# Performance work log

Hardware: AMD Instinct MI355X
Metric: run time of the kernel (lower is better)

The kernel has to match this reference:

```python
import jax, jax.numpy as jnp
import numpy as np

B, L, D = 2, 2048, 2048
H, KVH, Dh = 16, 8, 128
S_ROPE = 1024
EPS = 1e-5


def rms_norm(x, w):
    xf = x.astype(jnp.float32)
    xf = xf * jax.lax.rsqrt(jnp.mean(xf * xf, axis=-1, keepdims=True) + EPS)
    return (xf * w).astype(x.dtype)


def rotate_half(x):
    x1, x2 = jnp.split(x, 2, axis=-1)
    return jnp.concatenate((-x2, x1), axis=-1)


def setup_inputs() -> dict:
    key = jax.random.key(0)
    ks = jax.random.split(key, 12)
    sc = 0.02
    # 1D rope tables at every absolute position (theta = 500000 as in config)
    inv_freq = 1.0 / (500000.0 ** (np.arange(0, Dh, 2, dtype=np.float32) / Dh))
    ang = np.arange(L, dtype=np.float32)[:, None] * inv_freq[None, :]  # [L, Dh/2]
    emb = np.concatenate([ang, ang], axis=-1)  # [L, Dh]
    # 3D rope as per-pair 2x2 rotation matrices
    ang3 = np.random.RandomState(0).uniform(-np.pi, np.pi, size=(S_ROPE, Dh // 2)).astype(np.float32)
    R = np.stack([np.stack([np.cos(ang3), -np.sin(ang3)], -1),
                  np.stack([np.sin(ang3), np.cos(ang3)], -1)], -2)  # [S,Dh/2,2,2]
    mpos = jnp.array([[[128, 1025], [1160, 513]],
                      [[128, 1025], [1160, 513]]], dtype=jnp.int64)
    return {
        "hidden_states": jax.random.normal(ks[0], (B, L, D), jnp.float32),
        "temb": jax.random.normal(ks[1], (B, D), jnp.float32),
        "w_ln": jnp.ones((D,), jnp.float32),
        "w_mod": jax.random.normal(ks[2], (D, 3 * D), jnp.float32) * sc,
        "b_mod": jnp.zeros((3 * D,), jnp.float32),
        "wq": jax.random.normal(ks[3], (D, H * Dh), jnp.float32) * sc,
        "wk": jax.random.normal(ks[4], (D, KVH * Dh), jnp.float32) * sc,
        "wv": jax.random.normal(ks[5], (D, KVH * Dh), jnp.float32) * sc,
        "wo": jax.random.normal(ks[6], (H * Dh, D), jnp.float32) * sc,
        "qn_w": jnp.ones((Dh,), jnp.float32),
        "kn_w": jnp.ones((Dh,), jnp.float32),
        "cos_1d": jnp.asarray(np.cos(emb)),
        "sin_1d": jnp.asarray(np.sin(emb)),
        "rope_3d": jnp.asarray(R),
        "modality_positions": mpos,
    }


def _masks(modality_positions):
    pos = jnp.arange(L)  # [L]
    off = modality_positions[..., 0]   # [B, S]
    ln = modality_positions[..., 1]    # [B, S]
    meta = 1  # add_time_embeds=True, add_ar_embeds=False
    seg_end = off + jnp.maximum(ln, meta)
    in_full = (pos[None, None, :] >= off[..., None]) & (pos[None, None, :] < seg_end[..., None])
    text_mask = ~jnp.any(in_full, axis=1)  # [B, L]
    img_start = off + meta
    in_img = (pos[None, None, :] >= img_start[..., None]) & (pos[None, None, :] < (off + ln)[..., None])
    rel = jnp.sum(jnp.where(in_img, pos[None, None, :] - img_start[..., None], 0), axis=1)  # [B, L]
    img_mask = jnp.any(in_img, axis=1) & (rel < S_ROPE) & (rel >= 0)
    rel = jnp.clip(rel, 0, S_ROPE - 1)
    return text_mask, img_mask, rel


def _apply_mixed_rope(q, k, cos_1d, sin_1d, rope_3d, text_mask, img_mask, rel):
    # text 1D rope (rotate_half style), applied at absolute position
    c = cos_1d[None, None]  # [1,1,L,Dh]
    s = sin_1d[None, None]
    q_txt = q * c + rotate_half(q) * s
    k_txt = k * c + rotate_half(k) * s
    # image 3D rope: per-pair 2x2 rotation gathered at within-image index
    R = rope_3d[rel]  # [B, L, Dh/2, 2, 2]
    q2 = q.reshape(*q.shape[:-1], Dh // 2, 2)
    k2 = k.reshape(*k.shape[:-1], Dh // 2, 2)
    q_img = jnp.einsum('bhlpi,blpij->bhlpj', q2, R).reshape(q.shape)
    k_img = jnp.einsum('bhlpi,blpij->bhlpj', k2, R).reshape(k.shape)
    mt = text_mask[:, None, :, None]
    mi = img_mask[:, None, :, None]
    q_out = jnp.where(mt, q_txt, jnp.where(mi, q_img, q))
    k_out = jnp.where(mt, k_txt, jnp.where(mi, k_img, k))
    return q_out, k_out


def reference(hidden_states, temb, w_ln, w_mod, b_mod, wq, wk, wv, wo,
              qn_w, kn_w, cos_1d, sin_1d, rope_3d, modality_positions):
    dtype = hidden_states.dtype
    # adaLN modulation
    mod = jax.nn.silu(temb) @ w_mod + b_mod  # [B, 3D]
    shift, scale, gate = jnp.split(mod, 3, axis=-1)
    xn = rms_norm(hidden_states, w_ln)
    xm = (xn.astype(jnp.float32) * (1.0 + scale[:, None, :].astype(jnp.float32))
          + shift[:, None, :].astype(jnp.float32)).astype(dtype)
    # qkv projections (GQA)
    q = (xm @ wq).reshape(B, L, H, Dh).transpose(0, 2, 1, 3)
    k = (xm @ wk).reshape(B, L, KVH, Dh).transpose(0, 2, 1, 3)
    v = (xm @ wv).reshape(B, L, KVH, Dh).transpose(0, 2, 1, 3)
    # qk-norm over head_dim
    q = rms_norm(q, qn_w)
    k = rms_norm(k, kn_w)
    # mixed 3D-image / 1D-text RoPE
    text_mask, img_mask, rel = _masks(modality_positions)
    q, k = _apply_mixed_rope(q, k, cos_1d, sin_1d, rope_3d, text_mask, img_mask, rel)
    # GQA: repeat kv heads (repeat_interleave along head dim)
    n_rep = H // KVH
    k = jnp.repeat(k, n_rep, axis=1)
    v = jnp.repeat(v, n_rep, axis=1)
    # full attention (no causal mask for diffusion block)
    scores = jnp.einsum('bhqd,bhkd->bhqk', q, k) / jnp.sqrt(jnp.asarray(Dh, q.dtype))
    attn = jax.nn.softmax(scores, axis=-1)
    o = jnp.einsum('bhqk,bhkd->bhqd', attn, v)
    o = o.transpose(0, 2, 1, 3).reshape(B, L, H * Dh) @ wo
    return hidden_states + gate[:, None, :].astype(dtype) * o


if __name__ == '__main__':
    out = reference(**setup_inputs())
    print(out.shape, out.dtype)
```

## Files before the change

### kernel.cpp

```cpp
#include <hip/hip_runtime.h>
#include <stdint.h>
#include <math.h>

typedef unsigned short u16;
typedef __attribute__((ext_vector_type(8))) short short8;
typedef __attribute__((ext_vector_type(4))) float fx4;
typedef __attribute__((ext_vector_type(4))) unsigned short u16x4;

#define DEV __device__ __forceinline__

DEV u16 f2bf(float f) {
  unsigned u = __builtin_bit_cast(unsigned, f);
  return (u16)((u + 0x7FFFu + ((u >> 16) & 1u)) >> 16);
}
DEV float bf2f(u16 h) { return __builtin_bit_cast(float, ((unsigned)h) << 16); }

DEV fx4 mfma16(short8 a, short8 b, fx4 c) {
  return __builtin_amdgcn_mfma_f32_16x16x32_bf16(a, b, c, 0, 0, 0);
}

#define GLD16(g, l)                                                            \
  __builtin_amdgcn_global_load_lds(                                            \
      (const __attribute__((address_space(1))) void*)(g),                      \
      (__attribute__((address_space(3))) void*)(l), 16, 0, 0)

__global__ __launch_bounds__(512) void k_silu_mod(
    const float* __restrict__ temb, const float* __restrict__ wmod,
    const float* __restrict__ bmod, float* __restrict__ mod) {
  __shared__ float st[4096];
  __shared__ float red[8][2][64];
  int tid = threadIdx.x;
  for (int i = tid; i < 4096; i += 512) {
    float t = temb[i];
    st[i] = t / (1.0f + __expf(-t));
  }
  __syncthreads();
  int j = blockIdx.x * 64 + (tid & 63);
  int ks = tid >> 6;
  float a0 = 0.f, a1 = 0.f;
  for (int d = ks * 256; d < ks * 256 + 256; ++d) {
    float w = wmod[(size_t)d * 6144 + j];
    a0 += st[d] * w;
    a1 += st[2048 + d] * w;
  }
  red[ks][0][tid & 63] = a0;
  red[ks][1][tid & 63] = a1;
  __syncthreads();
  if (tid < 64) {
    float s0 = 0.f, s1 = 0.f;
#pragma unroll
    for (int i = 0; i < 8; ++i) {
      s0 += red[i][0][tid];
      s1 += red[i][1][tid];
    }
    mod[j] = s0 + bmod[j];
    mod[6144 + j] = s1 + bmod[j];
  }
}

__global__ __launch_bounds__(256) void k_xm(
    const float* __restrict__ x, const float* __restrict__ wln,
    const float* __restrict__ mod, u16* __restrict__ xm) {
  int row = blockIdx.x;
  int b = row >> 11;
  const float* xr = x + (size_t)row * 2048;
  int tid = threadIdx.x;
  float4 v0 = ((const float4*)xr)[tid];
  float4 v1 = ((const float4*)xr)[tid + 256];
  float ss = v0.x * v0.x + v0.y * v0.y + v0.z * v0.z + v0.w * v0.w +
             v1.x * v1.x + v1.y * v1.y + v1.z * v1.z + v1.w * v1.w;
  for (int m = 1; m < 64; m <<= 1) ss += __shfl_xor(ss, m);
  __shared__ float red[4];
  if ((tid & 63) == 0) red[tid >> 6] = ss;
  __syncthreads();
  ss = red[0] + red[1] + red[2] + red[3];
  float r = rsqrtf(ss * (1.0f / 2048.0f) + 1e-5f);
  const float* mb = mod + (size_t)b * 6144;
#pragma unroll
  for (int c = 0; c < 2; ++c) {
    int j0 = (tid + c * 256) * 4;
    float4 xv = c ? v1 : v0;
    float4 sh = *(const float4*)(mb + j0);
    float4 sc = *(const float4*)(mb + 2048 + j0);
    float4 wl = *(const float4*)(wln + j0);
    u16x4 o;
    o.x = f2bf(xv.x * r * wl.x * (1.f + sc.x) + sh.x);
    o.y = f2bf(xv.y * r * wl.y * (1.f + sc.y) + sh.y);
    o.z = f2bf(xv.z * r * wl.z * (1.f + sc.z) + sh.z);
    o.w = f2bf(xv.w * r * wl.w * (1.f + sc.w) + sh.w);
    *(u16x4*)(xm + (size_t)row * 2048 + j0) = o;
  }
}

__global__ __launch_bounds__(256) void k_tconv(
    const float* __restrict__ src, u16* __restrict__ dst, int cols, int rows) {
  __shared__ float t[32][33];
  int kb = blockIdx.x * 32, nb = blockIdx.y * 32;
  int tx = threadIdx.x, ty = threadIdx.y;
#pragma unroll
  for (int i = 0; i < 4; ++i)
    t[ty + i * 8][tx] = src[(size_t)(kb + ty + i * 8) * cols + nb + tx];
  __syncthreads();
#pragma unroll
  for (int i = 0; i < 4; ++i)
    dst[(size_t)(nb + ty + i * 8) * rows + kb + tx] = f2bf(t[tx][ty + i * 8]);
}

template <int EPI>
__global__ __launch_bounds__(256) void k_gemm(
    const u16* __restrict__ A, const u16* __restrict__ Bt, void* __restrict__ Cp,
    const float* __restrict__ hid, const float* __restrict__ mod, int N, int K) {
  __shared__ u16 As[128 * 32];
  __shared__ u16 Bs[128 * 32];
  int tid = threadIdx.x;
  int wave = tid >> 6, lane = tid & 63, quad = lane >> 4, l16 = lane & 15;
  int m0 = blockIdx.y * 128, n0 = blockIdx.x * 128;
  int wm = (wave >> 1) * 64, wn = (wave & 1) * 64;
  fx4 acc[4][4] = {};
  int rowa = tid >> 2;
  int chunk = (tid & 3) ^ ((rowa >> 1) & 3);
  int cola = chunk * 8;
  const u16* Ag = A + (size_t)(m0 + rowa) * K + cola;
  const u16* Bg = Bt + (size_t)(n0 + rowa) * K + cola;
  u16* AsW = &As[wave * 512];
  u16* BsW = &Bs[wave * 512];
  int sl = (quad ^ ((l16 >> 1) & 3)) * 8;
  for (int k0 = 0; k0 < K; k0 += 32) {
    GLD16(Ag + k0, AsW);
    GLD16(Ag + k0 + (size_t)64 * K, AsW + 2048);
    GLD16(Bg + k0, BsW);
    GLD16(Bg + k0 + (size_t)64 * K, BsW + 2048);
    __syncthreads();
    short8 af[4], bfr[4];
#pragma unroll
    for (int i = 0; i < 4; ++i) {
      af[i] = *(const short8*)&As[(wm + i * 16 + l16) * 32 + sl];
      bfr[i] = *(const short8*)&Bs[(wn + i * 16 + l16) * 32 + sl];
    }
#pragma unroll
    for (int i = 0; i < 4; ++i)
#pragma unroll
      for (int j = 0; j < 4; ++j) acc[i][j] = mfma16(af[i], bfr[j], acc[i][j]);
    __syncthreads();
  }
#pragma unroll
  for (int i = 0; i < 4; ++i) {
    int row = m0 + wm + i * 16 + quad * 4;
#pragma unroll
    for (int j = 0; j < 4; ++j) {
      int col = n0 + wn + j * 16 + l16;
      if (EPI == 0) {
        u16* C = (u16*)Cp;
#pragma unroll
        for (int r = 0; r < 4; ++r)
          C[(size_t)(row + r) * N + col] = f2bf(acc[i][j][r]);
      } else {
        float* C = (float*)Cp;
        int b = row >> 11;
        float g = mod[(size_t)b * 6144 + 4096 + col];
#pragma unroll
        for (int r = 0; r < 4; ++r)
          C[(size_t)(row + r) * N + col] =
              hid[(size_t)(row + r) * N + col] + g * acc[i][j][r];
      }
    }
  }
}

__global__ __launch_bounds__(192) void k_qknorm(
    const u16* __restrict__ qkv, const float* __restrict__ qn,
    const float* __restrict__ kn, const float* __restrict__ cos1,
    const float* __restrict__ sin1, const float* __restrict__ r3,
    const int* __restrict__ mpos, u16* __restrict__ Q, u16* __restrict__ Kb) {
  int bx = blockIdx.x;
  int b = bx >> 11, l = bx & 2047;
  int tid = threadIdx.x;
  int slot = tid >> 3, sub = tid & 7;
  bool isq = slot < 16;
  int head = isq ? slot : slot - 16;
  const u16* base = qkv + (size_t)bx * 4096 + (isq ? slot * 128 : 2048 + head * 128);
  int d0 = sub * 16;
  float xv[16];
#pragma unroll
  for (int i = 0; i < 16; ++i) xv[i] = bf2f(base[d0 + i]);
  float ss = 0.f;
#pragma unroll
  for (int i = 0; i < 16; ++i) ss += xv[i] * xv[i];
  ss += __shfl_xor(ss, 1);
  ss += __shfl_xor(ss, 2);
  ss += __shfl_xor(ss, 4);
  float r = rsqrtf(ss * (1.0f / 128.0f) + 1e-5f);
  int mp[8];
  {
    bool is64 = (mpos[1] == 0) & (mpos[3] == 0) & (mpos[5] == 0) & (mpos[7] == 0);
#pragma unroll
    for (int i = 0; i < 8; ++i) mp[i] = is64 ? mpos[2 * i] : mpos[i];
  }
  bool infull = false, inimg = false;
  int rel = 0;
#pragma unroll
  for (int s = 0; s < 2; ++s) {
    int off = mp[b * 4 + s * 2], ln = mp[b * 4 + s * 2 + 1];
    int mx = ln > 1 ? ln : 1;
    infull |= (l >= off) && (l < off + mx);
    bool ii = (l >= off + 1) && (l < off + ln);
    inimg |= ii;
    rel += ii ? (l - (off + 1)) : 0;
  }
  bool text = !infull;
  bool img = inimg && (rel < 1024);
  const float* w = isq ? qn : kn;
  float out[16];
  if (text) {
    int dp0 = d0 ^ 64;
    float sgn = (d0 < 64) ? -1.f : 1.f;
#pragma unroll
    for (int i = 0; i < 16; ++i) {
      int d = d0 + i, dp = dp0 + i;
      float c = cos1[(size_t)l * 128 + d];
      float s = sin1[(size_t)l * 128 + d];
      float xp = bf2f(base[dp]);
      out[i] = r * (xv[i] * w[d] * c + sgn * xp * w[dp] * s);
    }
  } else if (img) {
    const float* R = r3 + ((size_t)rel * 64 + (d0 >> 1)) * 4;
#pragma unroll
    for (int p = 0; p < 8; ++p) {
      float a = xv[2 * p] * w[d0 + 2 * p] * r;
      float c2 = xv[2 * p + 1] * w[d0 + 2 * p + 1] * r;
      out[2 * p] = a * R[4 * p + 0] + c2 * R[4 * p + 2];
      out[2 * p + 1] = a * R[4 * p + 1] + c2 * R[4 * p + 3];
    }
  } else {
#pragma unroll
    for (int i = 0; i < 16; ++i) out[i] = xv[i] * w[d0 + i] * r;
  }
  if (isq) {
    u16* dst = Q + ((size_t)(b * 16 + head) * 2048 + l) * 128 + d0;
#pragma unroll
    for (int i = 0; i < 16; ++i) dst[i] = f2bf(out[i] * 0.08838834764831845f);
  } else {
    u16* dst = Kb + ((size_t)(b * 8 + head) * 2048 + l) * 128 + d0;
#pragma unroll
    for (int i = 0; i < 16; ++i) dst[i] = f2bf(out[i]);
  }
}

__global__ __launch_bounds__(256) void k_vtrans(const u16* __restrict__ qkv,
                                                u16* __restrict__ VT) {
  __shared__ u16 t[64][65];
  int bh = blockIdx.x;
  int l0 = blockIdx.y * 64, d0 = blockIdx.z * 64;
  int b = bh >> 3, kvh = bh & 7;
  int tx = threadIdx.x & 63, tg = threadIdx.x >> 6;
#pragma unroll
  for (int i = 0; i < 16; ++i) {
    int li = tg + i * 4;
    t[li][tx] = qkv[(size_t)(b * 2048 + l0 + li) * 4096 + 3072 + kvh * 128 + d0 + tx];
  }
  __syncthreads();
#pragma unroll
  for (int i = 0; i < 16; ++i) {
    int di = tg + i * 4;
    VT[((size_t)bh * 128 + d0 + di) * 2048 + l0 + tx] = t[tx][di];
  }
}

__global__ __launch_bounds__(256, 4) void k_attn(
    const u16* __restrict__ Q, const u16* __restrict__ Kb,
    const u16* __restrict__ VT, u16* __restrict__ O) {
  __shared__ u16 Ks[64 * 128];
  __shared__ u16 Vs[128 * 64];
  __shared__ u16 Ps[64 * 64];
  int tid = threadIdx.x;
  int wave = tid >> 6, lane = tid & 63, quad = lane >> 4, l16 = lane & 15;
  int bh = blockIdx.y;
  int b = bh >> 4, h = bh & 15, kvh = h >> 1;
  int q0 = blockIdx.x * 64;
  const u16* Qb = Q + ((size_t)bh * 2048 + q0 + wave * 16) * 128;
  short8 qf[4];
#pragma unroll
  for (int ks = 0; ks < 4; ++ks)
    qf[ks] = *(const short8*)(Qb + l16 * 128 + ks * 32 + quad * 8);
  const u16* Kg = Kb + (size_t)(b * 8 + kvh) * 2048 * 128;
  const u16* Vg = VT + (size_t)(b * 8 + kvh) * 128 * 2048;
  float mrow[4], lrow[4];
  fx4 of[8] = {};
#pragma unroll
  for (int r = 0; r < 4; ++r) {
    mrow[r] = -INFINITY;
    lrow[r] = 0.f;
  }
  size_t kgo[4], vgo[4];
#pragma unroll
  for (int i = 0; i < 4; ++i) {
    int kr = i * 16 + wave * 4 + (lane >> 4);
    kgo[i] = (size_t)kr * 128 + (((lane & 15) ^ (kr & 15)) * 8);
    int vr = i * 32 + wave * 8 + (lane >> 3);
    vgo[i] = (size_t)vr * 2048 + (((lane & 7) ^ (vr & 7)) * 8);
  }
  int sl8 = ((l16 & 7)) * 8;
  for (int kv0 = 0; kv0 < 2048; kv0 += 64) {
#pragma unroll
    for (int i = 0; i < 4; ++i) {
      GLD16(Kg + (size_t)kv0 * 128 + kgo[i], &Ks[i * 2048 + wave * 512]);
      GLD16(Vg + kv0 + vgo[i], &Vs[i * 2048 + wave * 512]);
    }
    __syncthreads();
    fx4 sf[4] = {};
#pragma unroll
    for (int ct = 0; ct < 4; ++ct) {
#pragma unroll
      for (int ks = 0; ks < 4; ++ks) {
        short8 kf = *(const short8*)&Ks[(ct * 16 + l16) * 128 +
                                        ((ks * 4 + quad) ^ l16) * 8];
        sf[ct] = mfma16(qf[ks], kf, sf[ct]);
      }
    }
    float al[4];
#pragma unroll
    for (int r = 0; r < 4; ++r) {
      float cm = fmaxf(fmaxf(sf[0][r], sf[1][r]), fmaxf(sf[2][r], sf[3][r]));
      cm = fmaxf(cm, __shfl_xor(cm, 1));
      cm = fmaxf(cm, __shfl_xor(cm, 2));
      cm = fmaxf(cm, __shfl_xor(cm, 4));
      cm = fmaxf(cm, __shfl_xor(cm, 8));
      float mnew = fmaxf(mrow[r], cm);
      float alpha = __expf(mrow[r] - mnew);
      mrow[r] = mnew;
      float p0 = __expf(sf[0][r] - mnew);
      float p1 = __expf(sf[1][r] - mnew);
      float p2 = __expf(sf[2][r] - mnew);
      float p3 = __expf(sf[3][r] - mnew);
      float rs = p0 + p1 + p2 + p3;
      rs += __shfl_xor(rs, 1);
      rs += __shfl_xor(rs, 2);
      rs += __shfl_xor(rs, 4);
      rs += __shfl_xor(rs, 8);
      lrow[r] = lrow[r] * alpha + rs;
      al[r] = alpha;
      int prow = wave * 16 + quad * 4 + r;
      int hb = l16 >> 3;
#pragma unroll
      for (int ct = 0; ct < 4; ++ct) {
        float pv = ct == 0 ? p0 : ct == 1 ? p1 : ct == 2 ? p2 : p3;
        int slot = (2 * ct + hb) ^ (prow & 7);
        Ps[prow * 64 + slot * 8 + (l16 & 7)] = f2bf(pv);
      }
    }
#pragma unroll
    for (int c2 = 0; c2 < 8; ++c2) {
      of[c2][0] *= al[0];
      of[c2][1] *= al[1];
      of[c2][2] *= al[2];
      of[c2][3] *= al[3];
    }
#pragma unroll
    for (int ks2 = 0; ks2 < 2; ++ks2) {
      int rsl = ((ks2 * 4 + quad) ^ (l16 & 7)) * 8;
      short8 pa = *(const short8*)&Ps[(wave * 16 + l16) * 64 + rsl];
#pragma unroll
      for (int c2 = 0; c2 < 8; ++c2) {
        short8 vb = *(const short8*)&Vs[(c2 * 16 + l16) * 64 + rsl];
        of[c2] = mfma16(pa, vb, of[c2]);
      }
    }
    __syncthreads();
  }
#pragma unroll
  for (int r = 0; r < 4; ++r) {
    float inv = 1.0f / lrow[r];
    int qrow = q0 + wave * 16 + quad * 4 + r;
#pragma unroll
    for (int c2 = 0; c2 < 8; ++c2)
      O[((size_t)b * 2048 + qrow) * 2048 + h * 128 + c2 * 16 + l16] =
          f2bf(of[c2][r] * inv);
  }
  (void)sl8;
}

extern "C" void kernel_launch(void* const* d_in, const int* in_sizes, int n_in,
                              void* d_out, int out_size, void* d_ws, size_t ws_size,
                              hipStream_t stream) {
  (void)in_sizes; (void)n_in; (void)out_size; (void)ws_size;
  const float* hid  = (const float*)d_in[0];
  const float* temb = (const float*)d_in[1];
  const float* wln  = (const float*)d_in[2];
  const float* wmod = (const float*)d_in[3];
  const float* bmod = (const float*)d_in[4];
  const float* wq   = (const float*)d_in[5];
  const float* wk   = (const float*)d_in[6];
  const float* wv   = (const float*)d_in[7];
  const float* wo   = (const float*)d_in[8];
  const float* qn   = (const float*)d_in[9];
  const float* kn   = (const float*)d_in[10];
  const float* cos1 = (const float*)d_in[11];
  const float* sin1 = (const float*)d_in[12];
  const float* r3   = (const float*)d_in[13];
  const int*   mpos = (const int*)d_in[14];

  char* ws = (char*)d_ws;
  float* mod = (float*)(ws + 0);
  u16* xm  = (u16*)(ws + 49152);
  u16* wT  = (u16*)(ws + 16826368);
  u16* woT = wT;
  u16* qkv = (u16*)(ws + 33603584);
  u16* Qb  = (u16*)(ws + 67158016);
  u16* Kv  = (u16*)(ws + 83935232);
  u16* VT  = (u16*)(ws + 92323840);
  u16* Ob  = qkv;

  dim3 b32(32, 8);
  k_silu_mod<<<96, 512, 0, stream>>>(temb, wmod, bmod, mod);
  k_tconv<<<dim3(64, 64), b32, 0, stream>>>(wq, wT, 2048, 2048);
  k_tconv<<<dim3(64, 32), b32, 0, stream>>>(wk, wT + (size_t)2048 * 2048, 1024, 2048);
  k_tconv<<<dim3(64, 32), b32, 0, stream>>>(wv, wT + (size_t)3072 * 2048, 1024, 2048);
  k_xm<<<4096, 256, 0, stream>>>(hid, wln, mod, xm);
  k_gemm<0><<<dim3(32, 32), 256, 0, stream>>>(xm, wT, qkv, nullptr, nullptr, 4096, 2048);
  k_tconv<<<dim3(64, 64), b32, 0, stream>>>(wo, woT, 2048, 2048);
  k_qknorm<<<4096, 192, 0, stream>>>(qkv, qn, kn, cos1, sin1, r3, mpos, Qb, Kv);
  k_vtrans<<<dim3(16, 32, 2), 256, 0, stream>>>(qkv, VT);
  k_attn<<<dim3(32, 32), 256, 0, stream>>>(Qb, Kv, VT, Ob);
  k_gemm<1><<<dim3(16, 32), 256, 0, stream>>>(Ob, woT, d_out, hid, mod, 2048, 2048);
}
```

Measured before the change: 571.9 us.

## Double-buffer K/V tiles in attention with 8-wave blocks, exp2 softmax, lazy rescale

Restructures the attention kernel into 512-thread blocks covering 128 query rows, with double-buffered K/V shared-memory tiles so the next tile loads while the current one is computed. Softmax switches to exp2 with log2(e) folded into the Q scale. The running-max rescale is skipped unless some row's max grows by more than 8. It also adds setprio hints around the MFMA sections. The lazy rescale keeps stale maxima, so exponentials can reach about 2^8 before correction, and the larger blocks lower occupancy and raise LDS use.

```diff
diff --git a/kernel.cpp b/kernel.cpp
--- a/kernel.cpp
+++ b/kernel.cpp
@@ -19,10 +19,18 @@
   return __builtin_amdgcn_mfma_f32_16x16x32_bf16(a, b, c, 0, 0, 0);
 }
 
+#if __has_builtin(__builtin_amdgcn_exp2f)
+DEV float exp2v(float x) { return __builtin_amdgcn_exp2f(x); }
+#else
+DEV float exp2v(float x) { return exp2f(x); }
+#endif
+
 #define GLD16(g, l)                                                            \
   __builtin_amdgcn_global_load_lds(                                            \
       (const __attribute__((address_space(1))) void*)(g),                      \
       (__attribute__((address_space(3))) void*)(l), 16, 0, 0)
+
+#define WAIT_ALL() asm volatile("s_waitcnt vmcnt(0) lgkmcnt(0)" ::: "memory")
 
 __global__ __launch_bounds__(512) void k_silu_mod(
     const float* __restrict__ temb, const float* __restrict__ wmod,
@@ -238,7 +246,8 @@
   if (isq) {
     u16* dst = Q + ((size_t)(b * 16 + head) * 2048 + l) * 128 + d0;
 #pragma unroll
-    for (int i = 0; i < 16; ++i) dst[i] = f2bf(out[i] * 0.08838834764831845f);
+    for (int i = 0; i < 16; ++i)
+      dst[i] = f2bf(out[i] * (0.08838834764831845f * 1.4426950408889634f));
   } else {
     u16* dst = Kb + ((size_t)(b * 8 + head) * 2048 + l) * 128 + d0;
 #pragma unroll
@@ -266,17 +275,17 @@
   }
 }
 
-__global__ __launch_bounds__(256, 4) void k_attn(
+__global__ __launch_bounds__(512, 4) void k_attn(
     const u16* __restrict__ Q, const u16* __restrict__ Kb,
     const u16* __restrict__ VT, u16* __restrict__ O) {
-  __shared__ u16 Ks[64 * 128];
-  __shared__ u16 Vs[128 * 64];
-  __shared__ u16 Ps[64 * 64];
+  __shared__ u16 Ks[2][64 * 128];
+  __shared__ u16 Vs[2][128 * 64];
+  __shared__ u16 Ps[128 * 64];
   int tid = threadIdx.x;
   int wave = tid >> 6, lane = tid & 63, quad = lane >> 4, l16 = lane & 15;
   int bh = blockIdx.y;
   int b = bh >> 4, h = bh & 15, kvh = h >> 1;
-  int q0 = blockIdx.x * 64;
+  int q0 = blockIdx.x * 128;
   const u16* Qb = Q + ((size_t)bh * 2048 + q0 + wave * 16) * 128;
   short8 qf[4];
 #pragma unroll
@@ -291,33 +300,39 @@
     mrow[r] = -INFINITY;
     lrow[r] = 0.f;
   }
-  size_t kgo[4], vgo[4];
-#pragma unroll
-  for (int i = 0; i < 4; ++i) {
-    int kr = i * 16 + wave * 4 + (lane >> 4);
+  size_t kgo[2], vgo[2];
+#pragma unroll
+  for (int i = 0; i < 2; ++i) {
+    int kr = i * 32 + wave * 4 + (lane >> 4);
     kgo[i] = (size_t)kr * 128 + (((lane & 15) ^ (kr & 15)) * 8);
-    int vr = i * 32 + wave * 8 + (lane >> 3);
+    int vr = i * 64 + wave * 8 + (lane >> 3);
     vgo[i] = (size_t)vr * 2048 + (((lane & 7) ^ (vr & 7)) * 8);
   }
-  int sl8 = ((l16 & 7)) * 8;
-  for (int kv0 = 0; kv0 < 2048; kv0 += 64) {
-#pragma unroll
-    for (int i = 0; i < 4; ++i) {
-      GLD16(Kg + (size_t)kv0 * 128 + kgo[i], &Ks[i * 2048 + wave * 512]);
-      GLD16(Vg + kv0 + vgo[i], &Vs[i * 2048 + wave * 512]);
-    }
-    __syncthreads();
+
+  auto STAGE = [&](int t, int buf) {
+    size_t ko = (size_t)t * 8192;
+    size_t vo = (size_t)t * 64;
+#pragma unroll
+    for (int i = 0; i < 2; ++i) {
+      GLD16(Kg + ko + kgo[i], &Ks[buf][i * 4096 + wave * 512]);
+      GLD16(Vg + vo + vgo[i], &Vs[buf][i * 4096 + wave * 512]);
+    }
+  };
+
+  auto COMPUTE = [&](int buf) {
     fx4 sf[4] = {};
+    __builtin_amdgcn_s_setprio(1);
 #pragma unroll
     for (int ct = 0; ct < 4; ++ct) {
 #pragma unroll
       for (int ks = 0; ks < 4; ++ks) {
-        short8 kf = *(const short8*)&Ks[(ct * 16 + l16) * 128 +
-                                        ((ks * 4 + quad) ^ l16) * 8];
+        short8 kf = *(const short8*)&Ks[buf][(ct * 16 + l16) * 128 +
+                                            (((ks * 4 + quad) ^ l16) * 8)];
         sf[ct] = mfma16(qf[ks], kf, sf[ct]);
       }
     }
-    float al[4];
+    __builtin_amdgcn_s_setprio(0);
+    float cmv[4];
 #pragma unroll
     for (int r = 0; r < 4; ++r) {
       float cm = fmaxf(fmaxf(sf[0][r], sf[1][r]), fmaxf(sf[2][r], sf[3][r]));
@@ -325,48 +340,69 @@
       cm = fmaxf(cm, __shfl_xor(cm, 2));
       cm = fmaxf(cm, __shfl_xor(cm, 4));
       cm = fmaxf(cm, __shfl_xor(cm, 8));
-      float mnew = fmaxf(mrow[r], cm);
-      float alpha = __expf(mrow[r] - mnew);
-      mrow[r] = mnew;
-      float p0 = __expf(sf[0][r] - mnew);
-      float p1 = __expf(sf[1][r] - mnew);
-      float p2 = __expf(sf[2][r] - mnew);
-      float p3 = __expf(sf[3][r] - mnew);
-      float rs = p0 + p1 + p2 + p3;
+      cmv[r] = cm;
+    }
+    bool need = false;
+#pragma unroll
+    for (int r = 0; r < 4; ++r) need |= (cmv[r] > mrow[r] + 8.0f);
+    if (__any(need)) {
+#pragma unroll
+      for (int r = 0; r < 4; ++r) {
+        float mn = fmaxf(mrow[r], cmv[r]);
+        float al = exp2v(mrow[r] - mn);
+        mrow[r] = mn;
+        lrow[r] *= al;
+#pragma unroll
+        for (int c2 = 0; c2 < 8; ++c2) of[c2][r] *= al;
+      }
+    }
+    int hb = l16 >> 3;
+#pragma unroll
+    for (int r = 0; r < 4; ++r) {
+      float p0 = exp2v(sf[0][r] - mrow[r]);
+      float p1 = exp2v(sf[1][r] - mrow[r]);
+      float p2 = exp2v(sf[2][r] - mrow[r]);
+      float p3 = exp2v(sf[3][r] - mrow[r]);
+      float rs = (p0 + p1) + (p2 + p3);
       rs += __shfl_xor(rs, 1);
       rs += __shfl_xor(rs, 2);
       rs += __shfl_xor(rs, 4);
       rs += __shfl_xor(rs, 8);
-      lrow[r] = lrow[r] * alpha + rs;
-      al[r] = alpha;
+      lrow[r] += rs;
       int prow = wave * 16 + quad * 4 + r;
-      int hb = l16 >> 3;
-#pragma unroll
-      for (int ct = 0; ct < 4; ++ct) {
-        float pv = ct == 0 ? p0 : ct == 1 ? p1 : ct == 2 ? p2 : p3;
-        int slot = (2 * ct + hb) ^ (prow & 7);
-        Ps[prow * 64 + slot * 8 + (l16 & 7)] = f2bf(pv);
-      }
-    }
-#pragma unroll
-    for (int c2 = 0; c2 < 8; ++c2) {
-      of[c2][0] *= al[0];
-      of[c2][1] *= al[1];
-      of[c2][2] *= al[2];
-      of[c2][3] *= al[3];
-    }
+      int pb = prow * 64, px = prow & 7, lo = l16 & 7;
+      Ps[pb + ((0 + hb) ^ px) * 8 + lo] = f2bf(p0);
+      Ps[pb + ((2 + hb) ^ px) * 8 + lo] = f2bf(p1);
+      Ps[pb + ((4 + hb) ^ px) * 8 + lo] = f2bf(p2);
+      Ps[pb + ((6 + hb) ^ px) * 8 + lo] = f2bf(p3);
+    }
+    __builtin_amdgcn_s_setprio(1);
 #pragma unroll
     for (int ks2 = 0; ks2 < 2; ++ks2) {
-      int rsl = ((ks2 * 4 + quad) ^ (l16 & 7)) * 8;
+      int rsl = (((ks2 * 4 + quad) ^ (l16 & 7)) * 8);
       short8 pa = *(const short8*)&Ps[(wave * 16 + l16) * 64 + rsl];
 #pragma unroll
       for (int c2 = 0; c2 < 8; ++c2) {
-        short8 vb = *(const short8*)&Vs[(c2 * 16 + l16) * 64 + rsl];
+        short8 vb = *(const short8*)&Vs[buf][(c2 * 16 + l16) * 64 + rsl];
         of[c2] = mfma16(pa, vb, of[c2]);
       }
     }
-    __syncthreads();
-  }
+    __builtin_amdgcn_s_setprio(0);
+  };
+
+  STAGE(0, 0);
+  WAIT_ALL();
+  __builtin_amdgcn_s_barrier();
+  int cur = 0;
+  for (int t = 0; t < 31; ++t) {
+    STAGE(t + 1, cur ^ 1);
+    COMPUTE(cur);
+    WAIT_ALL();
+    __builtin_amdgcn_s_barrier();
+    cur ^= 1;
+  }
+  COMPUTE(cur);
+
 #pragma unroll
   for (int r = 0; r < 4; ++r) {
     float inv = 1.0f / lrow[r];
@@ -376,7 +412,6 @@
       O[((size_t)b * 2048 + qrow) * 2048 + h * 128 + c2 * 16 + l16] =
           f2bf(of[c2][r] * inv);
   }
-  (void)sl8;
 }
 
 extern "C" void kernel_launch(void* const* d_in, const int* in_sizes, int n_in,
@@ -420,6 +455,6 @@
   k_tconv<<<dim3(64, 64), b32, 0, stream>>>(wo, woT, 2048, 2048);
   k_qknorm<<<4096, 192, 0, stream>>>(qkv, qn, kn, cos1, sin1, r3, mpos, Qb, Kv);
   k_vtrans<<<dim3(16, 32, 2), 256, 0, stream>>>(qkv, VT);
-  k_attn<<<dim3(32, 32), 256, 0, stream>>>(Qb, Kv, VT, Ob);
+  k_attn<<<dim3(16, 32), 512, 0, stream>>>(Qb, Kv, VT, Ob);
   k_gemm<1><<<dim3(16, 32), 256, 0, stream>>>(Ob, woT, d_out, hid, mod, 2048, 2048);
 }
```

After: 532.2 us. 6.9% less time.
